# Kernel optimization log

Hardware: AMD Instinct MI355X
Metric: run time of the kernel (lower is better)

The kernel has to match this reference:

```python
import jax, jax.numpy as jnp
import numpy as np

B, N, E = 2, 2048, 1024
H = 16
D = E // H  # head_dim = 64
MLP = 4096
EPS = 1e-5


def _layernorm(x, g, b):
    mu = jnp.mean(x, axis=-1, keepdims=True)
    var = jnp.var(x, axis=-1, keepdims=True)
    return (x - mu) * jax.lax.rsqrt(var + EPS) * g + b


def setup_inputs() -> dict:
    key = jax.random.key(0)
    ks = jax.random.split(key, 12)
    s_e = 1.0 / np.sqrt(E)
    s_m = 1.0 / np.sqrt(MLP)
    return {
        "x": jax.random.normal(ks[0], (B, N, E), jnp.float32),
        "w_qkv": jax.random.uniform(ks[1], (E, 3 * E), jnp.float32, -s_e, s_e),
        "b_qkv": jax.random.uniform(ks[2], (3 * E,), jnp.float32, -s_e, s_e),
        "w_proj": jax.random.uniform(ks[3], (E, E), jnp.float32, -s_e, s_e),
        "b_proj": jax.random.uniform(ks[4], (E,), jnp.float32, -s_e, s_e),
        "g1": jnp.ones((E,), jnp.float32),
        "beta1": jnp.zeros((E,), jnp.float32),
        "g2": jnp.ones((E,), jnp.float32),
        "beta2": jnp.zeros((E,), jnp.float32),
        "w_fc1": jax.random.uniform(ks[5], (E, MLP), jnp.float32, -s_e, s_e),
        "b_fc1": jax.random.uniform(ks[6], (MLP,), jnp.float32, -s_e, s_e),
        "w_fc2": jax.random.uniform(ks[7], (MLP, E), jnp.float32, -s_m, s_m),
        "b_fc2": jax.random.uniform(ks[8], (E,), jnp.float32, -s_m, s_m),
    }


def reference(x, w_qkv, b_qkv, w_proj, b_proj, g1, beta1, g2, beta2,
              w_fc1, b_fc1, w_fc2, b_fc2):
    scale = D ** (-0.5)
    # --- attention block (pre-norm) ---
    h = _layernorm(x, g1, beta1)
    qkv = (h @ w_qkv + b_qkv).reshape(B, N, 3, H, D)
    q, k, v = (qkv[:, :, i].transpose(0, 2, 1, 3) for i in range(3))  # [B,H,N,D]
    scores = jnp.einsum("bhnd,bhmd->bhnm", q, k) * scale  # [B,H,N,N]
    attn = jax.nn.softmax(scores, axis=-1)
    out = jnp.einsum("bhnm,bhmd->bhnd", attn, v)
    out = out.transpose(0, 2, 1, 3).reshape(B, N, E)
    x = x + (out @ w_proj + b_proj)
    # --- MLP block (pre-norm, exact GELU as in torch default) ---
    h = _layernorm(x, g2, beta2)
    h = jax.nn.gelu(h @ w_fc1 + b_fc1, approximate=False) @ w_fc2 + b_fc2
    return x + h
```

## Files before the change

kernel.cpp:

```cpp
#include <hip/hip_runtime.h>
#include <hip/hip_bf16.h>
#include <cmath>


typedef __hip_bfloat16 bf16;
typedef __bf16 bf16x8 __attribute__((ext_vector_type(8)));
typedef __bf16 bf16x4v __attribute__((ext_vector_type(4)));
typedef float  f32x4  __attribute__((ext_vector_type(4)));

#define CB 2
#define CN 2048
#define CE 1024
#define CH 16
#define CD 64
#define CMLP 4096
#define CM (CB*CN)

#define PS 136

__device__ __forceinline__ float b2f(bf16 v){ return __bfloat162float(v); }
__device__ __forceinline__ bf16  f2b(float v){ return __float2bfloat16(v); }

__device__ __forceinline__ void gl_lds16(const void* g, void* l){
  __builtin_amdgcn_global_load_lds((__attribute__((address_space(1))) void*)g,
                                   (__attribute__((address_space(3))) void*)l,
                                   16, 0, 0);
}

__global__ __launch_bounds__(256) void transpose_k(const float* __restrict__ in,
                                                   bf16* __restrict__ out,
                                                   int K, int N){
  __shared__ float tile[32][33];
  const int n0 = blockIdx.x*32, k0 = blockIdx.y*32;
  const int tx = threadIdx.x & 31;
  const int ty = threadIdx.x >> 5;
  #pragma unroll
  for(int i=0;i<32;i+=8) tile[ty+i][tx] = in[(size_t)(k0+ty+i)*N + n0+tx];
  __syncthreads();
  #pragma unroll
  for(int i=0;i<32;i+=8) out[(size_t)(n0+ty+i)*K + k0+tx] = f2b(tile[tx][ty+i]);
}

__global__ __launch_bounds__(256) void ln_k(const float* __restrict__ x,
                                            const float* __restrict__ g,
                                            const float* __restrict__ be,
                                            bf16* __restrict__ out){
  const int row = blockIdx.x;
  const int t = threadIdx.x;
  const float4 v4 = ((const float4*)(x + (size_t)row*CE))[t];
  float v[4] = {v4.x, v4.y, v4.z, v4.w};
  float s=0.f, s2=0.f;
  #pragma unroll
  for(int i=0;i<4;i++){ s+=v[i]; s2+=v[i]*v[i]; }
  #pragma unroll
  for(int off=32; off>0; off>>=1){ s += __shfl_down(s,off); s2 += __shfl_down(s2,off); }
  __shared__ float red[8];
  __shared__ float mu_s, rs_s;
  const int wv=t>>6, ln=t&63;
  if(ln==0){ red[wv]=s; red[4+wv]=s2; }
  __syncthreads();
  if(t==0){
    float S=red[0]+red[1]+red[2]+red[3], S2=red[4]+red[5]+red[6]+red[7];
    float mu=S/CE;
    mu_s=mu; rs_s=rsqrtf(S2/CE - mu*mu + 1e-5f);
  }
  __syncthreads();
  const float mu=mu_s, rs=rs_s;
  #pragma unroll
  for(int i=0;i<4;i++){
    int c=t*4+i;
    out[(size_t)row*CE+c] = f2b((v[i]-mu)*rs*g[c] + be[c]);
  }
}

#define EP_QKV 0
#define EP_RES 1
#define EP_GELU 2

template<int MODE, int BN>
__global__ __launch_bounds__(256,2) void gemm_k(
  const bf16* __restrict__ A, const bf16* __restrict__ BT,
  const float* __restrict__ bias, const float* __restrict__ res,
  float* __restrict__ Cf, bf16* __restrict__ Cb,
  bf16* __restrict__ Cq, bf16* __restrict__ Ck, bf16* __restrict__ Cv,
  int Ksz, int Nsz)
{
  constexpr int NJ = BN/32;
  __shared__ __align__(16) bf16 Alds[2][128*64];
  __shared__ __align__(16) bf16 Blds[2][BN*64];
  const int tid = threadIdx.x;
  const int wave = tid>>6, lane = tid&63;
  const int m16 = lane&15, quad = lane>>4;
  const int wi = wave>>1, wj = wave&1;

  const int lin = blockIdx.x + gridDim.x*blockIdx.y;
  const int m_idx = (lin&7) + 8*((lin>>3)&3);
  const int n_idx = lin>>5;
  const size_t m0 = (size_t)m_idx*128;
  const size_t n0 = (size_t)n_idx*BN;

  f32x4 acc[4][NJ] = {};

  const int srow8 = lane>>3;
  const int schk  = ((lane&7)^srow8)*8;
  const bf16* pA = A  + (m0 + 32*wave      + srow8)*(size_t)Ksz + schk;
  const bf16* pB = BT + (n0 + (BN/4)*wave  + srow8)*(size_t)Ksz + schk;

  auto stage = [&](int buf, const bf16* gA, const bf16* gB){
    bf16* lA = &Alds[buf][wave*2048];
    bf16* lB = &Blds[buf][wave*(BN*16)];
    #pragma unroll
    for(int j=0;j<4;j++)  gl_lds16(gA + (size_t)(j*8)*Ksz, lA + j*512);
    #pragma unroll
    for(int j=0;j<NJ;j++) gl_lds16(gB + (size_t)(j*8)*Ksz, lB + j*512);
  };
  auto compute = [&](int buf){
    #pragma unroll
    for(int w=0;w<2;w++){
      const int sw = (m16&7);
      bf16x8 af[4], bfr[NJ];
      #pragma unroll
      for(int i=0;i<4;i++){
        const int row = wi*64+16*i+m16;
        af[i] = *(const bf16x8*)(&Alds[buf][row*64 + ((w*4+quad)^sw)*8]);
      }
      #pragma unroll
      for(int j=0;j<NJ;j++){
        const int row = wj*(BN/2)+16*j+m16;
        bfr[j] = *(const bf16x8*)(&Blds[buf][row*64 + ((w*4+quad)^sw)*8]);
      }
      #pragma unroll
      for(int i=0;i<4;i++)
        #pragma unroll
        for(int j=0;j<NJ;j++)
          acc[i][j] = __builtin_amdgcn_mfma_f32_16x16x32_bf16(af[i], bfr[j], acc[i][j], 0,0,0);
    }
  };

  const int kIters = Ksz/64;
  stage(0, pA, pB); pA += 64; pB += 64;
  for(int kb=0; kb<kIters; ++kb){
    __syncthreads();
    if(kb+1<kIters){ stage((kb+1)&1, pA, pB); pA += 64; pB += 64; }
    compute(kb&1);
  }

  #pragma unroll
  for(int i=0;i<4;i++){
    #pragma unroll
    for(int j=0;j<NJ;j++){
      const int col = (int)n0 + wj*(BN/2) + 16*j + m16;
      const float bcol = bias[col];
      #pragma unroll
      for(int r=0;r<4;r++){
        const int row = (int)m0 + wi*64 + 16*i + quad*4 + r;
        float v = acc[i][j][r] + bcol;
        if constexpr (MODE==EP_QKV){
          const int b = row>>11, n = row&2047;
          const int which = col>>10, cc = col&1023;
          const int h = cc>>6, d = cc&63;
          if(which==0)      Cq[(((size_t)(b*CH+h))*CN+n)*CD + d] = f2b(v);
          else if(which==1) Ck[(((size_t)(b*CH+h))*CN+n)*CD + d] = f2b(v);
          else              Cv[(((size_t)(b*CH+h))*CD+d)*CN + n] = f2b(v);
        } else if constexpr (MODE==EP_RES){
          v += res[(size_t)row*Nsz+col];
          Cf[(size_t)row*Nsz+col] = v;
        } else {
          const float u2 = 1.5957691216f*(v + 0.044715f*v*v*v);
          v = v * (1.f/(1.f + __expf(-u2)));
          Cb[(size_t)row*Nsz+col] = f2b(v);
        }
      }
    }
  }
}

__global__ __launch_bounds__(256,2) void attn_k(
  const bf16* __restrict__ Q, const bf16* __restrict__ Kx,
  const bf16* __restrict__ Vt, bf16* __restrict__ O)
{
  const int bh = blockIdx.y;
  const int b = bh>>4, h = bh&15;
  const int tid = threadIdx.x;
  const int wave = tid>>6, lane = tid&63;
  const int m16 = lane&15, quad = lane>>4;
  const int sw = m16&7;
  const int q0 = blockIdx.x*128 + wave*32;

  const bf16* Qb = Q  + (size_t)bh*CN*CD;
  const bf16* Kb = Kx + (size_t)bh*CN*CD;
  const bf16* Vb = Vt + (size_t)bh*CD*CN;

  bf16x8 qf[2][2];
  #pragma unroll
  for(int g=0;g<2;g++){
    const bf16* qp = Qb + (size_t)(q0+g*16+m16)*CD + quad*8;
    qf[g][0] = *(const bf16x8*)(qp);
    qf[g][1] = *(const bf16x8*)(qp + 32);
  }

  float li[2] = {0.f, 0.f};
  f32x4 oacc[2][4] = {};

  __shared__ __align__(16) bf16 Klds[128*64];
  __shared__ __align__(16) bf16 Vlds[64*128];
  __shared__ __align__(16) bf16 Plds[4][32*PS];
  bf16* Pw = &Plds[wave][0];

  const int krow = wave*32 + (lane>>3);
  const int kchk = (lane&7) ^ (lane>>3);
  const bf16* pK = Kb + (size_t)krow*CD + kchk*8;
  const int vrow = wave*16 + (lane>>4);
  const bf16* pV[4];
  #pragma unroll
  for(int j=0;j<4;j++){
    const int ck = (lane&15) ^ ((j*4 + (lane>>4)) & 7);
    pV[j] = Vb + (size_t)(vrow + j*4)*CN + ck*8;
  }
  bf16* lK = Klds + wave*2048;
  bf16* lV = Vlds + wave*2048;

  for(int kt=0; kt<CN; kt+=128){
    __syncthreads();
    #pragma unroll
    for(int j=0;j<4;j++){
      gl_lds16(pK + (size_t)j*8*CD, lK + j*512);
      gl_lds16(pV[j],               lV + j*512);
      pV[j] += 128;
    }
    pK += (size_t)128*CD;
    __syncthreads();

    f32x4 sf0[8], sf1[8];
    #pragma unroll
    for(int f=0;f<8;f++){
      const bf16* kb = Klds + (f*16+m16)*64;
      bf16x8 k0 = *(const bf16x8*)(kb + ((quad   ^ sw)*8));
      bf16x8 k1 = *(const bf16x8*)(kb + (((quad+4)^ sw)*8));
      f32x4 t0 = {}, t1 = {};
      t0 = __builtin_amdgcn_mfma_f32_16x16x32_bf16(k0, qf[0][0], t0, 0,0,0);
      t0 = __builtin_amdgcn_mfma_f32_16x16x32_bf16(k1, qf[0][1], t0, 0,0,0);
      t1 = __builtin_amdgcn_mfma_f32_16x16x32_bf16(k0, qf[1][0], t1, 0,0,0);
      t1 = __builtin_amdgcn_mfma_f32_16x16x32_bf16(k1, qf[1][1], t1, 0,0,0);
      sf0[f]=t0; sf1[f]=t1;
    }
    #pragma unroll
    for(int f=0;f<8;f++){
      bf16x4v p0, p1;
      #pragma unroll
      for(int r=0;r<4;r++){
        float e0 = __expf(sf0[f][r]*0.125f); li[0]+=e0; p0[r]=(__bf16)e0;
        float e1 = __expf(sf1[f][r]*0.125f); li[1]+=e1; p1[r]=(__bf16)e1;
      }
      *(bf16x4v*)(Pw + (size_t)m16*PS       + f*16 + quad*4) = p0;
      *(bf16x4v*)(Pw + (size_t)(16+m16)*PS  + f*16 + quad*4) = p1;
    }
    asm volatile("s_waitcnt lgkmcnt(0)" ::: "memory");
    #pragma unroll
    for(int c=0;c<4;c++){
      const bf16x8 ap0 = *(const bf16x8*)(Pw + (size_t)m16*PS      + c*32 + quad*8);
      const bf16x8 ap1 = *(const bf16x8*)(Pw + (size_t)(16+m16)*PS + c*32 + quad*8);
      #pragma unroll
      for(int dt=0;dt<4;dt++){
        const int d = dt*16+m16;
        bf16x8 bv = *(const bf16x8*)(Vlds + d*128 + (((c*4+quad) ^ sw)*8));
        oacc[0][dt] = __builtin_amdgcn_mfma_f32_16x16x32_bf16(ap0, bv, oacc[0][dt], 0,0,0);
        oacc[1][dt] = __builtin_amdgcn_mfma_f32_16x16x32_bf16(ap1, bv, oacc[1][dt], 0,0,0);
      }
    }
  }
  #pragma unroll
  for(int g=0;g<2;g++){
    li[g] += __shfl_xor(li[g], 16);
    li[g] += __shfl_xor(li[g], 32);
  }
  #pragma unroll
  for(int g=0;g<2;g++){
    float linv[4];
    #pragma unroll
    for(int r=0;r<4;r++) linv[r] = 1.f / __shfl(li[g], quad*4+r);
    #pragma unroll
    for(int dt=0;dt<4;dt++){
      #pragma unroll
      for(int r=0;r<4;r++){
        const int row = q0 + g*16 + quad*4 + r;
        O[((size_t)(b*CN+row))*CE + h*CD + dt*16 + m16] = f2b(oacc[g][dt][r]*linv[r]);
      }
    }
  }
}

extern "C" void kernel_launch(void* const* d_in, const int* in_sizes, int n_in,
                              void* d_out, int out_size, void* d_ws, size_t ws_size,
                              hipStream_t stream)
{
  (void)in_sizes; (void)n_in; (void)out_size; (void)ws_size;
  const float* x     = (const float*)d_in[0];
  const float* w_qkv = (const float*)d_in[1];
  const float* b_qkv = (const float*)d_in[2];
  const float* w_proj= (const float*)d_in[3];
  const float* b_proj= (const float*)d_in[4];
  const float* g1    = (const float*)d_in[5];
  const float* be1   = (const float*)d_in[6];
  const float* g2    = (const float*)d_in[7];
  const float* be2   = (const float*)d_in[8];
  const float* w_fc1 = (const float*)d_in[9];
  const float* b_fc1 = (const float*)d_in[10];
  const float* w_fc2 = (const float*)d_in[11];
  const float* b_fc2 = (const float*)d_in[12];
  float* out = (float*)d_out;

  char* ws = (char*)d_ws;
  size_t off = 0;
  auto alloc = [&](size_t bytes)->char*{
    char* p = ws + off;
    off += (bytes + 255) & ~(size_t)255;
    return p;
  };
  bf16* wqkvT = (bf16*)alloc((size_t)3072*1024*2);
  bf16* wprojT= (bf16*)alloc((size_t)1024*1024*2);
  bf16* wfc1T = (bf16*)alloc((size_t)4096*1024*2);
  bf16* wfc2T = (bf16*)alloc((size_t)1024*4096*2);
  bf16* h1    = (bf16*)alloc((size_t)CM*CE*2);
  bf16* q     = (bf16*)alloc((size_t)CM*CE*2);
  bf16* kk    = (bf16*)alloc((size_t)CM*CE*2);
  bf16* vT    = (bf16*)alloc((size_t)CM*CE*2);
  bf16* aO    = (bf16*)alloc((size_t)CM*CE*2);
  float* x2   = (float*)alloc((size_t)CM*CE*4);
  bf16* hmlp  = q;

  transpose_k<<<dim3(3072/32,1024/32),256,0,stream>>>(w_qkv, wqkvT, 1024,3072);
  transpose_k<<<dim3(1024/32,1024/32),256,0,stream>>>(w_proj, wprojT,1024,1024);
  transpose_k<<<dim3(4096/32,1024/32),256,0,stream>>>(w_fc1, wfc1T, 1024,4096);
  transpose_k<<<dim3(1024/32,4096/32),256,0,stream>>>(w_fc2, wfc2T, 4096,1024);

  ln_k<<<CM,256,0,stream>>>(x, g1, be1, h1);
  gemm_k<EP_QKV,128><<<dim3(3072/128, CM/128),256,0,stream>>>(
      h1, wqkvT, b_qkv, nullptr, nullptr, nullptr, q, kk, vT, 1024, 3072);
  attn_k<<<dim3(CN/128, CB*CH),256,0,stream>>>(q, kk, vT, aO);
  gemm_k<EP_RES,64><<<dim3(1024/64, CM/128),256,0,stream>>>(
      aO, wprojT, b_proj, x, x2, nullptr, nullptr,nullptr,nullptr, 1024, 1024);
  ln_k<<<CM,256,0,stream>>>(x2, g2, be2, h1);
  gemm_k<EP_GELU,128><<<dim3(4096/128, CM/128),256,0,stream>>>(
      h1, wfc1T, b_fc1, nullptr, nullptr, hmlp, nullptr,nullptr,nullptr, 1024, 4096);
  gemm_k<EP_RES,64><<<dim3(1024/64, CM/128),256,0,stream>>>(
      hmlp, wfc2T, b_fc2, x2, out, nullptr, nullptr,nullptr,nullptr, 4096, 1024);
}
```

Before: 351.3 us.

## Use larger 512-thread GEMM tiles, add k128 residual GEMM, swizzle attention grid

Replaces the 256-thread GEMM with a 256x256-tile, 8-wave kernel for the QKV and FC1 projections. It also adds a separate 128x128 tile kernel with a K-step of 128 for the residual projections (attention output projection and FC2). The larger tiles raise arithmetic intensity and cut redundant global loads. The cost is more LDS and registers per block, and fewer blocks in the grid. Attention blocks are remapped so neighbouring blocks share a head for K/V cache reuse, and exp is switched to exp2 with a prescaled log2e constant.

```diff
diff --git a/kernel.cpp b/kernel.cpp
--- a/kernel.cpp
+++ b/kernel.cpp
@@ -17,6 +17,13 @@
 #define CM (CB*CN)
 
 #define PS 136
+
+#if __has_builtin(__builtin_amdgcn_exp2f)
+#define EXP2F __builtin_amdgcn_exp2f
+#else
+#define EXP2F exp2f
+#endif
+#define SM_SCALE_LOG2E 0.18033688011112042f
 
 __device__ __forceinline__ float b2f(bf16 v){ return __bfloat162float(v); }
 __device__ __forceinline__ bf16  f2b(float v){ return __float2bfloat16(v); }
@@ -74,65 +81,62 @@
 }
 
 #define EP_QKV 0
-#define EP_RES 1
 #define EP_GELU 2
 
-template<int MODE, int BN>
-__global__ __launch_bounds__(256,2) void gemm_k(
+template<int MODE>
+__global__ __launch_bounds__(512,2) void gemm256_k(
   const bf16* __restrict__ A, const bf16* __restrict__ BT,
-  const float* __restrict__ bias, const float* __restrict__ res,
-  float* __restrict__ Cf, bf16* __restrict__ Cb,
-  bf16* __restrict__ Cq, bf16* __restrict__ Ck, bf16* __restrict__ Cv,
-  int Ksz, int Nsz)
+  const float* __restrict__ bias,
+  bf16* __restrict__ Cb, bf16* __restrict__ Cq, bf16* __restrict__ Ck,
+  bf16* __restrict__ Cv, int Ksz, int Nsz)
 {
-  constexpr int NJ = BN/32;
-  __shared__ __align__(16) bf16 Alds[2][128*64];
-  __shared__ __align__(16) bf16 Blds[2][BN*64];
+  __shared__ __align__(16) bf16 Alds[2][256*64];
+  __shared__ __align__(16) bf16 Blds[2][256*64];
   const int tid = threadIdx.x;
   const int wave = tid>>6, lane = tid&63;
   const int m16 = lane&15, quad = lane>>4;
-  const int wi = wave>>1, wj = wave&1;
+  const int sw = m16&7;
+  const int wi = wave>>2, wj = wave&3;
 
   const int lin = blockIdx.x + gridDim.x*blockIdx.y;
-  const int m_idx = (lin&7) + 8*((lin>>3)&3);
-  const int n_idx = lin>>5;
-  const size_t m0 = (size_t)m_idx*128;
-  const size_t n0 = (size_t)n_idx*BN;
-
-  f32x4 acc[4][NJ] = {};
+  const int m_idx = (lin&7) + 8*((lin>>3)&1);
+  const int n_idx = lin>>4;
+  const size_t m0 = (size_t)m_idx*256;
+  const size_t n0 = (size_t)n_idx*256;
+
+  f32x4 acc[8][4] = {};
 
   const int srow8 = lane>>3;
   const int schk  = ((lane&7)^srow8)*8;
-  const bf16* pA = A  + (m0 + 32*wave      + srow8)*(size_t)Ksz + schk;
-  const bf16* pB = BT + (n0 + (BN/4)*wave  + srow8)*(size_t)Ksz + schk;
+  const bf16* pA = A  + (m0 + 32*wave + srow8)*(size_t)Ksz + schk;
+  const bf16* pB = BT + (n0 + 32*wave + srow8)*(size_t)Ksz + schk;
 
   auto stage = [&](int buf, const bf16* gA, const bf16* gB){
     bf16* lA = &Alds[buf][wave*2048];
-    bf16* lB = &Blds[buf][wave*(BN*16)];
-    #pragma unroll
-    for(int j=0;j<4;j++)  gl_lds16(gA + (size_t)(j*8)*Ksz, lA + j*512);
-    #pragma unroll
-    for(int j=0;j<NJ;j++) gl_lds16(gB + (size_t)(j*8)*Ksz, lB + j*512);
+    bf16* lB = &Blds[buf][wave*2048];
+    #pragma unroll
+    for(int j=0;j<4;j++) gl_lds16(gA + (size_t)(j*8)*Ksz, lA + j*512);
+    #pragma unroll
+    for(int j=0;j<4;j++) gl_lds16(gB + (size_t)(j*8)*Ksz, lB + j*512);
   };
   auto compute = [&](int buf){
     #pragma unroll
     for(int w=0;w<2;w++){
-      const int sw = (m16&7);
-      bf16x8 af[4], bfr[NJ];
-      #pragma unroll
-      for(int i=0;i<4;i++){
-        const int row = wi*64+16*i+m16;
+      bf16x8 af[8], bfr[4];
+      #pragma unroll
+      for(int i=0;i<8;i++){
+        const int row = wi*128+16*i+m16;
         af[i] = *(const bf16x8*)(&Alds[buf][row*64 + ((w*4+quad)^sw)*8]);
       }
       #pragma unroll
-      for(int j=0;j<NJ;j++){
-        const int row = wj*(BN/2)+16*j+m16;
+      for(int j=0;j<4;j++){
+        const int row = wj*64+16*j+m16;
         bfr[j] = *(const bf16x8*)(&Blds[buf][row*64 + ((w*4+quad)^sw)*8]);
       }
       #pragma unroll
-      for(int i=0;i<4;i++)
+      for(int i=0;i<8;i++)
         #pragma unroll
-        for(int j=0;j<NJ;j++)
+        for(int j=0;j<4;j++)
           acc[i][j] = __builtin_amdgcn_mfma_f32_16x16x32_bf16(af[i], bfr[j], acc[i][j], 0,0,0);
     }
   };
@@ -146,14 +150,14 @@
   }
 
   #pragma unroll
-  for(int i=0;i<4;i++){
-    #pragma unroll
-    for(int j=0;j<NJ;j++){
-      const int col = (int)n0 + wj*(BN/2) + 16*j + m16;
+  for(int i=0;i<8;i++){
+    #pragma unroll
+    for(int j=0;j<4;j++){
+      const int col = (int)n0 + wj*64 + 16*j + m16;
       const float bcol = bias[col];
       #pragma unroll
       for(int r=0;r<4;r++){
-        const int row = (int)m0 + wi*64 + 16*i + quad*4 + r;
+        const int row = (int)m0 + wi*128 + 16*i + quad*4 + r;
         float v = acc[i][j][r] + bcol;
         if constexpr (MODE==EP_QKV){
           const int b = row>>11, n = row&2047;
@@ -162,9 +166,6 @@
           if(which==0)      Cq[(((size_t)(b*CH+h))*CN+n)*CD + d] = f2b(v);
           else if(which==1) Ck[(((size_t)(b*CH+h))*CN+n)*CD + d] = f2b(v);
           else              Cv[(((size_t)(b*CH+h))*CD+d)*CN + n] = f2b(v);
-        } else if constexpr (MODE==EP_RES){
-          v += res[(size_t)row*Nsz+col];
-          Cf[(size_t)row*Nsz+col] = v;
         } else {
           const float u2 = 1.5957691216f*(v + 0.044715f*v*v*v);
           v = v * (1.f/(1.f + __expf(-u2)));
@@ -175,17 +176,106 @@
   }
 }
 
+__global__ __launch_bounds__(512,2) void gemm128_k(
+  const bf16* __restrict__ A, const bf16* __restrict__ BT,
+  const float* __restrict__ bias, const float* __restrict__ res,
+  float* __restrict__ Cf, int Ksz, int Nsz)
+{
+  __shared__ __align__(16) bf16 Alds[2][128*128];
+  __shared__ __align__(16) bf16 Blds[2][128*128];
+  const int tid = threadIdx.x;
+  const int wave = tid>>6, lane = tid&63;
+  const int m16 = lane&15, quad = lane>>4;
+  const int sw = m16&7;
+  const int wi = wave>>2, wj = wave&3;
+
+  const int lin = blockIdx.x + gridDim.x*blockIdx.y;
+  const int m_idx = (lin&7) + 8*((lin>>3)&3);
+  const int n_idx = lin>>5;
+  const size_t m0 = (size_t)m_idx*128;
+  const size_t n0 = (size_t)n_idx*128;
+
+  f32x4 acc[4][2] = {};
+
+  const int rl = lane>>4;
+  const int slot = lane&15;
+  const int sce = (slot&8) | ((slot^rl)&7);
+  const bf16* pAe = A  + (m0 + 16*wave + rl)*(size_t)Ksz + sce*8;
+  const bf16* pAo = A  + (m0 + 16*wave + rl)*(size_t)Ksz + (sce^4)*8;
+  const bf16* pBe = BT + (n0 + 16*wave + rl)*(size_t)Ksz + sce*8;
+  const bf16* pBo = BT + (n0 + 16*wave + rl)*(size_t)Ksz + (sce^4)*8;
+
+  auto stage = [&](int buf, size_t koff){
+    bf16* lA = &Alds[buf][wave*16*128];
+    bf16* lB = &Blds[buf][wave*16*128];
+    #pragma unroll
+    for(int j=0;j<4;j++){
+      const bf16* sA = ((j&1)?pAo:pAe) + koff + (size_t)(4*j)*Ksz;
+      const bf16* sB = ((j&1)?pBo:pBe) + koff + (size_t)(4*j)*Ksz;
+      gl_lds16(sA, lA + j*512);
+      gl_lds16(sB, lB + j*512);
+    }
+  };
+  auto compute = [&](int buf){
+    #pragma unroll
+    for(int w=0;w<4;w++){
+      bf16x8 af[4], bfr[2];
+      #pragma unroll
+      for(int i=0;i<4;i++){
+        const int row = wi*64+16*i+m16;
+        af[i] = *(const bf16x8*)(&Alds[buf][row*128 + ((w*4+quad)^sw)*8]);
+      }
+      #pragma unroll
+      for(int j=0;j<2;j++){
+        const int row = wj*32+16*j+m16;
+        bfr[j] = *(const bf16x8*)(&Blds[buf][row*128 + ((w*4+quad)^sw)*8]);
+      }
+      #pragma unroll
+      for(int i=0;i<4;i++)
+        #pragma unroll
+        for(int j=0;j<2;j++)
+          acc[i][j] = __builtin_amdgcn_mfma_f32_16x16x32_bf16(af[i], bfr[j], acc[i][j], 0,0,0);
+    }
+  };
+
+  const int kIters = Ksz/128;
+  size_t koff = 128;
+  stage(0, 0);
+  for(int kb=0; kb<kIters; ++kb){
+    __syncthreads();
+    if(kb+1<kIters){ stage((kb+1)&1, koff); koff += 128; }
+    compute(kb&1);
+  }
+
+  #pragma unroll
+  for(int i=0;i<4;i++){
+    #pragma unroll
+    for(int j=0;j<2;j++){
+      const int col = (int)n0 + wj*32 + 16*j + m16;
+      const float bcol = bias[col];
+      #pragma unroll
+      for(int r=0;r<4;r++){
+        const int row = (int)m0 + wi*64 + 16*i + quad*4 + r;
+        float v = acc[i][j][r] + bcol + res[(size_t)row*Nsz+col];
+        Cf[(size_t)row*Nsz+col] = v;
+      }
+    }
+  }
+}
+
 __global__ __launch_bounds__(256,2) void attn_k(
   const bf16* __restrict__ Q, const bf16* __restrict__ Kx,
   const bf16* __restrict__ Vt, bf16* __restrict__ O)
 {
-  const int bh = blockIdx.y;
+  const int lin = blockIdx.x + gridDim.x*blockIdx.y;
+  const int bh = (lin&7) + 8*(lin>>7);
+  const int qblk = (lin>>3)&15;
   const int b = bh>>4, h = bh&15;
   const int tid = threadIdx.x;
   const int wave = tid>>6, lane = tid&63;
   const int m16 = lane&15, quad = lane>>4;
   const int sw = m16&7;
-  const int q0 = blockIdx.x*128 + wave*32;
+  const int q0 = qblk*128 + wave*32;
 
   const bf16* Qb = Q  + (size_t)bh*CN*CD;
   const bf16* Kb = Kx + (size_t)bh*CN*CD;
@@ -249,8 +339,8 @@
       bf16x4v p0, p1;
       #pragma unroll
       for(int r=0;r<4;r++){
-        float e0 = __expf(sf0[f][r]*0.125f); li[0]+=e0; p0[r]=(__bf16)e0;
-        float e1 = __expf(sf1[f][r]*0.125f); li[1]+=e1; p1[r]=(__bf16)e1;
+        float e0 = EXP2F(sf0[f][r]*SM_SCALE_LOG2E); li[0]+=e0; p0[r]=(__bf16)e0;
+        float e1 = EXP2F(sf1[f][r]*SM_SCALE_LOG2E); li[1]+=e1; p1[r]=(__bf16)e1;
       }
       *(bf16x4v*)(Pw + (size_t)m16*PS       + f*16 + quad*4) = p0;
       *(bf16x4v*)(Pw + (size_t)(16+m16)*PS  + f*16 + quad*4) = p1;
@@ -335,14 +425,14 @@
   transpose_k<<<dim3(1024/32,4096/32),256,0,stream>>>(w_fc2, wfc2T, 4096,1024);
 
   ln_k<<<CM,256,0,stream>>>(x, g1, be1, h1);
-  gemm_k<EP_QKV,128><<<dim3(3072/128, CM/128),256,0,stream>>>(
-      h1, wqkvT, b_qkv, nullptr, nullptr, nullptr, q, kk, vT, 1024, 3072);
+  gemm256_k<EP_QKV><<<dim3(3072/256, CM/256),512,0,stream>>>(
+      h1, wqkvT, b_qkv, nullptr, q, kk, vT, 1024, 3072);
   attn_k<<<dim3(CN/128, CB*CH),256,0,stream>>>(q, kk, vT, aO);
-  gemm_k<EP_RES,64><<<dim3(1024/64, CM/128),256,0,stream>>>(
-      aO, wprojT, b_proj, x, x2, nullptr, nullptr,nullptr,nullptr, 1024, 1024);
+  gemm128_k<<<dim3(1024/128, CM/128),512,0,stream>>>(
+      aO, wprojT, b_proj, x, x2, 1024, 1024);
   ln_k<<<CM,256,0,stream>>>(x2, g2, be2, h1);
-  gemm_k<EP_GELU,128><<<dim3(4096/128, CM/128),256,0,stream>>>(
-      h1, wfc1T, b_fc1, nullptr, nullptr, hmlp, nullptr,nullptr,nullptr, 1024, 4096);
-  gemm_k<EP_RES,64><<<dim3(1024/64, CM/128),256,0,stream>>>(
-      hmlp, wfc2T, b_fc2, x2, out, nullptr, nullptr,nullptr,nullptr, 4096, 1024);
-}
+  gemm256_k<EP_GELU><<<dim3(4096/256, CM/256),512,0,stream>>>(
+      h1, wfc1T, b_fc1, hmlp, nullptr, nullptr, nullptr, 1024, 4096);
+  gemm128_k<<<dim3(1024/128, CM/128),512,0,stream>>>(
+      hmlp, wfc2T, b_fc2, x2, out, 4096, 1024);
+}
```

After: 366.8 us. 1.04x slower.
